# Kernel optimization log

Measured on AMD Instinct MI355X. Metric: run time of the kernel, lower is better.

The kernel has to match this reference:

```python
import jax, jax.numpy as jnp
import numpy as np

HEADS = 8
D_MODEL = 512
D_K = D_MODEL // HEADS
B, S = 2, 2048


def setup_inputs() -> dict:
    key = jax.random.key(0)
    ks = jax.random.split(key, 12)
    f = lambda k, shape: jax.random.normal(k, shape, dtype=jnp.float32)
    inp = {
        'q': f(ks[0], (B, S, D_MODEL)),
        'k': f(ks[1], (B, S, D_MODEL)),
        'v': f(ks[2], (B, S, D_MODEL)),
        'mask': jax.random.randint(ks[3], (B, S, S), 0, 2, dtype=jnp.int32),
        'Wq': f(ks[4], (D_MODEL, D_MODEL)) * 0.02,
        'bq': jnp.zeros((D_MODEL,), jnp.float32),
        'Wk': f(ks[5], (D_MODEL, D_MODEL)) * 0.02,
        'bk': jnp.zeros((D_MODEL,), jnp.float32),
        'Wv': f(ks[6], (D_MODEL, D_MODEL)) * 0.02,
        'bv': jnp.zeros((D_MODEL,), jnp.float32),
        'Wo': f(ks[7], (D_MODEL, D_MODEL)) * 0.02,
        'bo': jnp.zeros((D_MODEL,), jnp.float32),
    }
    return inp


def reference(q, k, v, mask, Wq, bq, Wk, bk, Wv, bv, Wo, bo):
    bs = q.shape[0]
    # linear projections then split heads: [B, H, S, D_K]
    qh = (q @ Wq + bq).reshape(bs, -1, HEADS, D_K).transpose(0, 2, 1, 3)
    kh = (k @ Wk + bk).reshape(bs, -1, HEADS, D_K).transpose(0, 2, 1, 3)
    vh = (v @ Wv + bv).reshape(bs, -1, HEADS, D_K).transpose(0, 2, 1, 3)
    # scores: [B, H, Sq, Sk]
    scores = jnp.einsum('bhqd,bhkd->bhqk', qh, kh) / jnp.sqrt(jnp.float32(D_K))
    scores = jnp.where(mask[:, None, :, :] == 0, jnp.float32(-10000.0), scores)
    attn = jax.nn.softmax(scores, axis=-1)
    # dropout p=0.0 -> identity (inference-equivalent)
    ctx = jnp.einsum('bhqk,bhkd->bhqd', attn, vh)
    concat = ctx.transpose(0, 2, 1, 3).reshape(bs, -1, D_MODEL)
    out = concat @ Wo + bo
    return (out, attn)
```

## Files before the change

### kernel.cpp

```cpp
#include <hip/hip_runtime.h>
#include <math.h>

#define HEADS 8
#define DK 64
#define DMODEL 512
#define BATCH 2
#define SEQ 2048
#define BH (BATCH * HEADS)

using f32x4 = __attribute__((ext_vector_type(4))) float;
using s16x8 = __attribute__((ext_vector_type(8))) short;
using fp16x2 = __attribute__((ext_vector_type(2))) __fp16;

union FragU {
  uint4 u;
  s16x8 s;
  unsigned short us[8];
};
union PkU {
  fp16x2 h;
  unsigned int u;
};

__device__ __forceinline__ unsigned short f32_to_bf16(float f) {
  unsigned int u = __float_as_uint(f);
  u += 0x7fffu + ((u >> 16) & 1u);
  return (unsigned short)(u >> 16);
}
__device__ __forceinline__ float bf16_to_f32(unsigned short h) {
  return __uint_as_float(((unsigned int)h) << 16);
}

__global__ __launch_bounds__(256) void pack_mask_kernel(
    const int* __restrict__ mask, unsigned int* __restrict__ bits) {
  const size_t row = blockIdx.x;
  const int wv = threadIdx.x >> 6, lane = threadIdx.x & 63;
  #pragma unroll
  for (int i = 0; i < 8; ++i) {
    const int c = wv * 512 + i * 64 + lane;
    unsigned long long bal = __ballot(mask[row * SEQ + c] != 0);
    if (lane == 0) {
      bits[row * 64 + (c >> 5)] = (unsigned int)bal;
      bits[row * 64 + (c >> 5) + 1] = (unsigned int)(bal >> 32);
    }
  }
}

__global__ __launch_bounds__(256) void wsplit4_kernel(
    const float* __restrict__ W0, const float* __restrict__ W1,
    const float* __restrict__ W2, const float* __restrict__ W3,
    unsigned short* __restrict__ WtHi4, unsigned short* __restrict__ WtLo4) {
  __shared__ float t[64][65];
  const int z = blockIdx.z;
  const float* W = (z == 0) ? W0 : (z == 1) ? W1 : (z == 2) ? W2 : W3;
  unsigned short* WtHi = WtHi4 + (size_t)z * (DMODEL * DMODEL);
  unsigned short* WtLo = WtLo4 + (size_t)z * (DMODEL * DMODEL);
  const int k0 = blockIdx.x * 64, n0 = blockIdx.y * 64;
  const int tid = threadIdx.x;
  const int r = tid >> 2, c = (tid & 3) * 16;
  #pragma unroll
  for (int e = 0; e < 4; ++e) {
    f32x4 v = *(const f32x4*)&W[(size_t)(k0 + r) * DMODEL + n0 + c + e * 4];
    #pragma unroll
    for (int j = 0; j < 4; ++j) t[r][c + e * 4 + j] = v[j];
  }
  __syncthreads();
  const int rn = tid >> 2, ck = (tid & 3) * 16;
  #pragma unroll
  for (int half = 0; half < 2; ++half) {
    FragU hi, lo;
    #pragma unroll
    for (int e = 0; e < 8; ++e) {
      float x = t[ck + half * 8 + e][rn];
      unsigned short h = f32_to_bf16(x);
      hi.us[e] = h;
      lo.us[e] = f32_to_bf16(x - bf16_to_f32(h));
    }
    const size_t o = (size_t)(n0 + rn) * DMODEL + k0 + ck + half * 8;
    *(uint4*)&WtHi[o] = hi.u;
    *(uint4*)&WtLo[o] = lo.u;
  }
}

template <int MODE>
__global__ __launch_bounds__(256) void proj_mfma_kernel(
    const float* __restrict__ X, const unsigned short* __restrict__ X16,
    const unsigned short* __restrict__ WtHi,
    const unsigned short* __restrict__ WtLo, const float* __restrict__ bias,
    float* __restrict__ Yf, unsigned short* __restrict__ Yhi,
    unsigned short* __restrict__ Ylo) {
  __shared__ unsigned short BsHi[64][72];
  __shared__ unsigned short BsLo[64][72];
  const int tid = threadIdx.x, wv = tid >> 6, lane = tid & 63;
  const int lr = lane & 15, lg = lane >> 4;
  const int m0 = blockIdx.x * 64;
  const int mw = m0 + wv * 16;
  const int n0 = blockIdx.y * 64;

  f32x4 acc[4] = {};
  for (int k0 = 0; k0 < 512; k0 += 64) {
    FragU ah[2], al[2];
    #pragma unroll
    for (int dc = 0; dc < 2; ++dc) {
      const size_t xi = (size_t)(mw + lr) * DMODEL + k0 + dc * 32 + lg * 8;
      if (MODE == 3) {
        ah[dc].u = *(const uint4*)&X16[xi];
      } else {
        f32x4 x0 = *(const f32x4*)&X[xi];
        f32x4 x1 = *(const f32x4*)&X[xi + 4];
        #pragma unroll
        for (int t = 0; t < 4; ++t) {
          unsigned short h0 = f32_to_bf16(x0[t]);
          unsigned short h1 = f32_to_bf16(x1[t]);
          ah[dc].us[t] = h0;
          ah[dc].us[4 + t] = h1;
          al[dc].us[t] = f32_to_bf16(x0[t] - bf16_to_f32(h0));
          al[dc].us[4 + t] = f32_to_bf16(x1[t] - bf16_to_f32(h1));
        }
      }
    }
    __syncthreads();
    #pragma unroll
    for (int e = 0; e < 2; ++e) {
      const int rr = (tid >> 3) + e * 32;
      const int cc = (tid & 7) * 8;
      *(uint4*)&BsHi[rr][cc] =
          *(const uint4*)&WtHi[(size_t)(n0 + rr) * DMODEL + k0 + cc];
      *(uint4*)&BsLo[rr][cc] =
          *(const uint4*)&WtLo[(size_t)(n0 + rr) * DMODEL + k0 + cc];
    }
    __syncthreads();
    #pragma unroll
    for (int jt = 0; jt < 4; ++jt) {
      #pragma unroll
      for (int dc = 0; dc < 2; ++dc) {
        FragU bh, bl;
        bh.u = *(const uint4*)&BsHi[jt * 16 + lr][dc * 32 + lg * 8];
        bl.u = *(const uint4*)&BsLo[jt * 16 + lr][dc * 32 + lg * 8];
        acc[jt] = __builtin_amdgcn_mfma_f32_16x16x32_bf16(ah[dc].s, bh.s, acc[jt], 0, 0, 0);
        acc[jt] = __builtin_amdgcn_mfma_f32_16x16x32_bf16(ah[dc].s, bl.s, acc[jt], 0, 0, 0);
        if (MODE != 3)
          acc[jt] = __builtin_amdgcn_mfma_f32_16x16x32_bf16(al[dc].s, bh.s, acc[jt], 0, 0, 0);
      }
    }
  }

  if (MODE == 3) {
    #pragma unroll
    for (int jt = 0; jt < 4; ++jt) {
      const int n = n0 + jt * 16 + lr;
      const float bi = bias[n];
      #pragma unroll
      for (int r = 0; r < 4; ++r)
        Yf[(size_t)(mw + lg * 4 + r) * DMODEL + n] = acc[jt][r] + bi;
    }
  } else {
    __syncthreads();
    #pragma unroll
    for (int jt = 0; jt < 4; ++jt) {
      const int n = jt * 16 + lr;
      const float bi = bias[n0 + n];
      #pragma unroll
      for (int r = 0; r < 4; ++r) {
        const float v = acc[jt][r] + bi;
        const int row = wv * 16 + lg * 4 + r;
        unsigned short hi = f32_to_bf16(v);
        BsHi[row][n] = hi;
        if (MODE == 1) BsLo[row][n] = f32_to_bf16(v - bf16_to_f32(hi));
      }
    }
    __syncthreads();
    if (MODE == 4) {
      const int b2 = m0 >> 11, s0 = m0 & 2047, hh = n0 >> 6;
      const int d = tid >> 2, sc = (tid & 3) * 16;
      #pragma unroll
      for (int e = 0; e < 16; ++e)
        Yhi[((size_t)(b2 * HEADS + hh) * DK + d) * SEQ + s0 + sc + e] =
            BsHi[sc + e][d];
    } else {
      #pragma unroll
      for (int p = 0; p < 2; ++p) {
        const int row = (tid >> 3) + p * 32;
        const int ch = (tid & 7) * 8;
        const size_t o = (size_t)(m0 + row) * DMODEL + n0 + ch;
        *(uint4*)&Yhi[o] = *(uint4*)&BsHi[row][ch];
        if (MODE == 1) *(uint4*)&Ylo[o] = *(uint4*)&BsLo[row][ch];
      }
    }
  }
}

__global__ __launch_bounds__(1024) void attn_fused_kernel(
    const unsigned short* __restrict__ Qhi, const unsigned short* __restrict__ Qlo,
    const unsigned short* __restrict__ Khi, const unsigned int* __restrict__ bits,
    const unsigned short* __restrict__ Vt, float* __restrict__ attn,
    unsigned short* __restrict__ ctx16) {
  __shared__ unsigned short pbuf[16][16 * 76];
  __shared__ float smred[16][16];
  const int id = blockIdx.x;
  const int xcd = id & 7, slot = id >> 3;
  const int bh = xcd + 8 * (slot & 1);
  const int qt = slot >> 1;
  const int b = bh >> 3, h = bh & 7;
  const int tid = threadIdx.x, wv = tid >> 6, lane = tid & 63;
  const int lr = lane & 15, lg = lane >> 4;
  const int q0 = qt * 16;
  const int kw = wv * 128;

  FragU qh[2], ql[2];
  #pragma unroll
  for (int dc = 0; dc < 2; ++dc) {
    const size_t qi = (size_t)(b * SEQ + q0 + lr) * DMODEL + h * DK + dc * 32 + lg * 8;
    qh[dc].u = *(const uint4*)&Qhi[qi];
    ql[dc].u = *(const uint4*)&Qlo[qi];
  }

  const float C = 0.125f * 1.44269504089f;
  PkU epk[8][2];
  float ls[4] = {0.f, 0.f, 0.f, 0.f};
  #pragma unroll
  for (int t = 0; t < 8; ++t) {
    FragU kh[2];
    #pragma unroll
    for (int dc = 0; dc < 2; ++dc) {
      const size_t kidx =
          (size_t)(b * SEQ + kw + t * 16 + lr) * DMODEL + h * DK + dc * 32 + lg * 8;
      kh[dc].u = *(const uint4*)&Khi[kidx];
    }
    f32x4 sa = {};
    #pragma unroll
    for (int dc = 0; dc < 2; ++dc) {
      sa = __builtin_amdgcn_mfma_f32_16x16x32_bf16(qh[dc].s, kh[dc].s, sa, 0, 0, 0);
      sa = __builtin_amdgcn_mfma_f32_16x16x32_bf16(ql[dc].s, kh[dc].s, sa, 0, 0, 0);
    }
    float ev[4];
    #pragma unroll
    for (int r = 0; r < 4; ++r) {
      const int q = q0 + lg * 4 + r;
      const unsigned int w = bits[((size_t)b * SEQ + q) * 64 + (kw >> 5) + (t >> 1)];
      const bool keep = (w >> (((t & 1) << 4) + lr)) & 1;
      const float e = keep ? exp2f(sa[r] * C) : 0.0f;
      ev[r] = e;
      ls[r] += e;
    }
    epk[t][0].h = __builtin_amdgcn_cvt_pkrtz(ev[0], ev[1]);
    epk[t][1].h = __builtin_amdgcn_cvt_pkrtz(ev[2], ev[3]);
  }

  #pragma unroll
  for (int r = 0; r < 4; ++r) {
    #pragma unroll
    for (int off = 1; off < 16; off <<= 1) ls[r] += __shfl_xor(ls[r], off);
    if (lr == 0) smred[wv][lg * 4 + r] = ls[r];
  }
  __syncthreads();
  float il[4];
  #pragma unroll
  for (int r = 0; r < 4; ++r) {
    float l = 0.f;
    #pragma unroll
    for (int w2 = 0; w2 < 16; ++w2) l += smred[w2][lg * 4 + r];
    il[r] = 1.0f / l;
  }

  unsigned short* pb = pbuf[wv];
  f32x4 acc[4] = {};
  #pragma unroll
  for (int c = 0; c < 2; ++c) {
    #pragma unroll
    for (int tt = 0; tt < 4; ++tt) {
      const int t = c * 4 + tt;
      float pv4[4];
      pv4[0] = (float)epk[t][0].h.x * il[0];
      pv4[1] = (float)epk[t][0].h.y * il[1];
      pv4[2] = (float)epk[t][1].h.x * il[2];
      pv4[3] = (float)epk[t][1].h.y * il[3];
      #pragma unroll
      for (int r = 0; r < 4; ++r) {
        const int q = q0 + lg * 4 + r;
        __builtin_nontemporal_store(
            pv4[r], &attn[((size_t)bh * SEQ + q) * SEQ + kw + t * 16 + lr]);
        pb[(lg * 4 + r) * 76 + tt * 16 + lr] = f32_to_bf16(pv4[r]);
      }
    }
    #pragma unroll
    for (int dc2 = 0; dc2 < 2; ++dc2) {
      FragU pa;
      pa.u = *(const uint4*)&pb[lr * 76 + dc2 * 32 + lg * 8];
      #pragma unroll
      for (int dt = 0; dt < 4; ++dt) {
        FragU bv;
        bv.u = *(const uint4*)&Vt[((size_t)bh * DK + dt * 16 + lr) * SEQ + kw +
                                  c * 64 + dc2 * 32 + lg * 8];
        acc[dt] = __builtin_amdgcn_mfma_f32_16x16x32_bf16(pa.s, bv.s, acc[dt], 0, 0, 0);
      }
    }
  }

  float* red = (float*)&pbuf[0][0];
  #pragma unroll 1
  for (int ofs = 8; ofs > 0; ofs >>= 1) {
    __syncthreads();
    if (wv >= ofs && wv < 2 * ofs) {
      float* dst = red + (size_t)(wv - ofs) * 1024;
      #pragma unroll
      for (int dt = 0; dt < 4; ++dt) *(f32x4*)&dst[dt * 256 + lane * 4] = acc[dt];
    }
    __syncthreads();
    if (wv < ofs) {
      const float* src = red + (size_t)wv * 1024;
      #pragma unroll
      for (int dt = 0; dt < 4; ++dt) acc[dt] += *(const f32x4*)&src[dt * 256 + lane * 4];
    }
  }
  if (wv == 0) {
    #pragma unroll
    for (int dt = 0; dt < 4; ++dt)
      #pragma unroll
      for (int r = 0; r < 4; ++r) {
        const int q = q0 + lg * 4 + r;
        ctx16[(size_t)(b * SEQ + q) * DMODEL + h * DK + dt * 16 + lr] =
            f32_to_bf16(acc[dt][r]);
      }
  }
}

extern "C" void kernel_launch(void* const* d_in, const int* in_sizes, int n_in,
                              void* d_out, int out_size, void* d_ws,
                              size_t ws_size, hipStream_t stream) {
  const float* q = (const float*)d_in[0];
  const float* k = (const float*)d_in[1];
  const float* v = (const float*)d_in[2];
  const int* mask = (const int*)d_in[3];
  const float* Wq = (const float*)d_in[4];
  const float* bq = (const float*)d_in[5];
  const float* Wk = (const float*)d_in[6];
  const float* bk = (const float*)d_in[7];
  const float* Wv = (const float*)d_in[8];
  const float* bv = (const float*)d_in[9];
  const float* Wo = (const float*)d_in[10];
  const float* bo = (const float*)d_in[11];

  float* out = (float*)d_out;
  float* attn = out + (size_t)BATCH * SEQ * DMODEL;

  char* w = (char*)d_ws;
  const size_t MB = 1u << 20;
  unsigned short* Qhi = (unsigned short*)(w + 0 * MB);
  unsigned short* Qlo = (unsigned short*)(w + 4 * MB);
  unsigned short* Khi = (unsigned short*)(w + 8 * MB);
  unsigned short* WtHi4 = (unsigned short*)(w + 12 * MB);
  unsigned short* WtLo4 = (unsigned short*)(w + 14 * MB);
  unsigned short* ctx16 = (unsigned short*)(w + 16 * MB);
  unsigned short* Vt = (unsigned short*)(w + 20 * MB);
  unsigned int* bits = (unsigned int*)(w + 24 * MB);

  const size_t WSTRIDE = (size_t)DMODEL * DMODEL;

  dim3 blk(256);
  pack_mask_kernel<<<dim3(BATCH * SEQ), blk, 0, stream>>>(mask, bits);

  wsplit4_kernel<<<dim3(8, 8, 4), blk, 0, stream>>>(Wq, Wk, Wv, Wo, WtHi4, WtLo4);

  proj_mfma_kernel<1><<<dim3(64, 8), blk, 0, stream>>>(
      q, nullptr, WtHi4 + 0 * WSTRIDE, WtLo4 + 0 * WSTRIDE, bq, nullptr, Qhi, Qlo);
  proj_mfma_kernel<2><<<dim3(64, 8), blk, 0, stream>>>(
      k, nullptr, WtHi4 + 1 * WSTRIDE, WtLo4 + 1 * WSTRIDE, bk, nullptr, Khi, nullptr);
  proj_mfma_kernel<4><<<dim3(64, 8), blk, 0, stream>>>(
      v, nullptr, WtHi4 + 2 * WSTRIDE, WtLo4 + 2 * WSTRIDE, bv, nullptr, Vt, nullptr);

  attn_fused_kernel<<<dim3(2048), dim3(1024), 0, stream>>>(Qhi, Qlo, Khi, bits,
                                                           Vt, attn, ctx16);

  proj_mfma_kernel<3><<<dim3(64, 8), blk, 0, stream>>>(
      nullptr, ctx16, WtHi4 + 3 * WSTRIDE, WtLo4 + 3 * WSTRIDE, bo, out, nullptr, nullptr);
}
```

Measured before the change: 251.1 us.

## Merge Q/K/V projections into one launch, preload mask words, use plain attn stores

The three separate Q, K and V projection launches become a single kernel that picks its input, weights and output layout from blockIdx.z. This removes two launches and lets the three projections fill the GPU together. In the attention kernel, each lane now loads its four mask words as one uint4 up front instead of issuing a scalar load per tile. The attention-probability stores switch from nontemporal to ordinary stores, which may change how the large attn write interacts with the cache.

Result: no change. 250.6 us, median of 2 (-0.2%).

```diff
diff --git a/kernel.cpp b/kernel.cpp
--- a/kernel.cpp
+++ b/kernel.cpp
@@ -82,13 +82,109 @@
   }
 }
 
-template <int MODE>
-__global__ __launch_bounds__(256) void proj_mfma_kernel(
-    const float* __restrict__ X, const unsigned short* __restrict__ X16,
-    const unsigned short* __restrict__ WtHi,
+__global__ __launch_bounds__(256) void proj_qkv_kernel(
+    const float* __restrict__ Xq, const float* __restrict__ Xk,
+    const float* __restrict__ Xv, const unsigned short* __restrict__ WtHi4,
+    const unsigned short* __restrict__ WtLo4, const float* __restrict__ bq,
+    const float* __restrict__ bk, const float* __restrict__ bv,
+    unsigned short* __restrict__ Qhi, unsigned short* __restrict__ Qlo,
+    unsigned short* __restrict__ Khi, unsigned short* __restrict__ Vt) {
+  __shared__ unsigned short BsHi[64][72];
+  __shared__ unsigned short BsLo[64][72];
+  const int z = blockIdx.z;
+  const float* X = (z == 0) ? Xq : (z == 1) ? Xk : Xv;
+  const float* bias = (z == 0) ? bq : (z == 1) ? bk : bv;
+  const unsigned short* WtHi = WtHi4 + (size_t)z * (DMODEL * DMODEL);
+  const unsigned short* WtLo = WtLo4 + (size_t)z * (DMODEL * DMODEL);
+
+  const int tid = threadIdx.x, wv = tid >> 6, lane = tid & 63;
+  const int lr = lane & 15, lg = lane >> 4;
+  const int m0 = blockIdx.x * 64;
+  const int mw = m0 + wv * 16;
+  const int n0 = blockIdx.y * 64;
+
+  f32x4 acc[4] = {};
+  for (int k0 = 0; k0 < 512; k0 += 64) {
+    FragU ah[2], al[2];
+    #pragma unroll
+    for (int dc = 0; dc < 2; ++dc) {
+      const size_t xi = (size_t)(mw + lr) * DMODEL + k0 + dc * 32 + lg * 8;
+      f32x4 x0 = *(const f32x4*)&X[xi];
+      f32x4 x1 = *(const f32x4*)&X[xi + 4];
+      #pragma unroll
+      for (int t = 0; t < 4; ++t) {
+        unsigned short h0 = f32_to_bf16(x0[t]);
+        unsigned short h1 = f32_to_bf16(x1[t]);
+        ah[dc].us[t] = h0;
+        ah[dc].us[4 + t] = h1;
+        al[dc].us[t] = f32_to_bf16(x0[t] - bf16_to_f32(h0));
+        al[dc].us[4 + t] = f32_to_bf16(x1[t] - bf16_to_f32(h1));
+      }
+    }
+    __syncthreads();
+    #pragma unroll
+    for (int e = 0; e < 2; ++e) {
+      const int rr = (tid >> 3) + e * 32;
+      const int cc = (tid & 7) * 8;
+      *(uint4*)&BsHi[rr][cc] =
+          *(const uint4*)&WtHi[(size_t)(n0 + rr) * DMODEL + k0 + cc];
+      *(uint4*)&BsLo[rr][cc] =
+          *(const uint4*)&WtLo[(size_t)(n0 + rr) * DMODEL + k0 + cc];
+    }
+    __syncthreads();
+    #pragma unroll
+    for (int jt = 0; jt < 4; ++jt) {
+      #pragma unroll
+      for (int dc = 0; dc < 2; ++dc) {
+        FragU bh, bl;
+        bh.u = *(const uint4*)&BsHi[jt * 16 + lr][dc * 32 + lg * 8];
+        bl.u = *(const uint4*)&BsLo[jt * 16 + lr][dc * 32 + lg * 8];
+        acc[jt] = __builtin_amdgcn_mfma_f32_16x16x32_bf16(ah[dc].s, bh.s, acc[jt], 0, 0, 0);
+        acc[jt] = __builtin_amdgcn_mfma_f32_16x16x32_bf16(ah[dc].s, bl.s, acc[jt], 0, 0, 0);
+        acc[jt] = __builtin_amdgcn_mfma_f32_16x16x32_bf16(al[dc].s, bh.s, acc[jt], 0, 0, 0);
+      }
+    }
+  }
+
+  __syncthreads();
+  #pragma unroll
+  for (int jt = 0; jt < 4; ++jt) {
+    const int n = jt * 16 + lr;
+    const float bi = bias[n0 + n];
+    #pragma unroll
+    for (int r = 0; r < 4; ++r) {
+      const float v = acc[jt][r] + bi;
+      const int row = wv * 16 + lg * 4 + r;
+      unsigned short hi = f32_to_bf16(v);
+      BsHi[row][n] = hi;
+      if (z == 0) BsLo[row][n] = f32_to_bf16(v - bf16_to_f32(hi));
+    }
+  }
+  __syncthreads();
+  if (z == 2) {
+    const int b2 = m0 >> 11, s0 = m0 & 2047, hh = n0 >> 6;
+    const int d = tid >> 2, sc = (tid & 3) * 16;
+    #pragma unroll
+    for (int e = 0; e < 16; ++e)
+      Vt[((size_t)(b2 * HEADS + hh) * DK + d) * SEQ + s0 + sc + e] =
+          BsHi[sc + e][d];
+  } else {
+    unsigned short* Yhi = (z == 0) ? Qhi : Khi;
+    #pragma unroll
+    for (int p = 0; p < 2; ++p) {
+      const int row = (tid >> 3) + p * 32;
+      const int ch = (tid & 7) * 8;
+      const size_t o = (size_t)(m0 + row) * DMODEL + n0 + ch;
+      *(uint4*)&Yhi[o] = *(uint4*)&BsHi[row][ch];
+      if (z == 0) *(uint4*)&Qlo[o] = *(uint4*)&BsLo[row][ch];
+    }
+  }
+}
+
+__global__ __launch_bounds__(256) void proj_out_kernel(
+    const unsigned short* __restrict__ X16, const unsigned short* __restrict__ WtHi,
     const unsigned short* __restrict__ WtLo, const float* __restrict__ bias,
-    float* __restrict__ Yf, unsigned short* __restrict__ Yhi,
-    unsigned short* __restrict__ Ylo) {
+    float* __restrict__ Yf) {
   __shared__ unsigned short BsHi[64][72];
   __shared__ unsigned short BsLo[64][72];
   const int tid = threadIdx.x, wv = tid >> 6, lane = tid & 63;
@@ -99,25 +195,11 @@
 
   f32x4 acc[4] = {};
   for (int k0 = 0; k0 < 512; k0 += 64) {
-    FragU ah[2], al[2];
+    FragU ah[2];
     #pragma unroll
     for (int dc = 0; dc < 2; ++dc) {
       const size_t xi = (size_t)(mw + lr) * DMODEL + k0 + dc * 32 + lg * 8;
-      if (MODE == 3) {
-        ah[dc].u = *(const uint4*)&X16[xi];
-      } else {
-        f32x4 x0 = *(const f32x4*)&X[xi];
-        f32x4 x1 = *(const f32x4*)&X[xi + 4];
-        #pragma unroll
-        for (int t = 0; t < 4; ++t) {
-          unsigned short h0 = f32_to_bf16(x0[t]);
-          unsigned short h1 = f32_to_bf16(x1[t]);
-          ah[dc].us[t] = h0;
-          ah[dc].us[4 + t] = h1;
-          al[dc].us[t] = f32_to_bf16(x0[t] - bf16_to_f32(h0));
-          al[dc].us[4 + t] = f32_to_bf16(x1[t] - bf16_to_f32(h1));
-        }
-      }
+      ah[dc].u = *(const uint4*)&X16[xi];
     }
     __syncthreads();
     #pragma unroll
@@ -139,54 +221,16 @@
         bl.u = *(const uint4*)&BsLo[jt * 16 + lr][dc * 32 + lg * 8];
         acc[jt] = __builtin_amdgcn_mfma_f32_16x16x32_bf16(ah[dc].s, bh.s, acc[jt], 0, 0, 0);
         acc[jt] = __builtin_amdgcn_mfma_f32_16x16x32_bf16(ah[dc].s, bl.s, acc[jt], 0, 0, 0);
-        if (MODE != 3)
-          acc[jt] = __builtin_amdgcn_mfma_f32_16x16x32_bf16(al[dc].s, bh.s, acc[jt], 0, 0, 0);
-      }
-    }
-  }
-
-  if (MODE == 3) {
-    #pragma unroll
-    for (int jt = 0; jt < 4; ++jt) {
-      const int n = n0 + jt * 16 + lr;
-      const float bi = bias[n];
-      #pragma unroll
-      for (int r = 0; r < 4; ++r)
-        Yf[(size_t)(mw + lg * 4 + r) * DMODEL + n] = acc[jt][r] + bi;
-    }
-  } else {
-    __syncthreads();
-    #pragma unroll
-    for (int jt = 0; jt < 4; ++jt) {
-      const int n = jt * 16 + lr;
-      const float bi = bias[n0 + n];
-      #pragma unroll
-      for (int r = 0; r < 4; ++r) {
-        const float v = acc[jt][r] + bi;
-        const int row = wv * 16 + lg * 4 + r;
-        unsigned short hi = f32_to_bf16(v);
-        BsHi[row][n] = hi;
-        if (MODE == 1) BsLo[row][n] = f32_to_bf16(v - bf16_to_f32(hi));
-      }
-    }
-    __syncthreads();
-    if (MODE == 4) {
-      const int b2 = m0 >> 11, s0 = m0 & 2047, hh = n0 >> 6;
-      const int d = tid >> 2, sc = (tid & 3) * 16;
-      #pragma unroll
-      for (int e = 0; e < 16; ++e)
-        Yhi[((size_t)(b2 * HEADS + hh) * DK + d) * SEQ + s0 + sc + e] =
-            BsHi[sc + e][d];
-    } else {
-      #pragma unroll
-      for (int p = 0; p < 2; ++p) {
-        const int row = (tid >> 3) + p * 32;
-        const int ch = (tid & 7) * 8;
-        const size_t o = (size_t)(m0 + row) * DMODEL + n0 + ch;
-        *(uint4*)&Yhi[o] = *(uint4*)&BsHi[row][ch];
-        if (MODE == 1) *(uint4*)&Ylo[o] = *(uint4*)&BsLo[row][ch];
-      }
-    }
+      }
+    }
+  }
+  #pragma unroll
+  for (int jt = 0; jt < 4; ++jt) {
+    const int n = n0 + jt * 16 + lr;
+    const float bi = bias[n];
+    #pragma unroll
+    for (int r = 0; r < 4; ++r)
+      Yf[(size_t)(mw + lg * 4 + r) * DMODEL + n] = acc[jt][r] + bi;
   }
 }
 
@@ -214,6 +258,12 @@
     qh[dc].u = *(const uint4*)&Qhi[qi];
     ql[dc].u = *(const uint4*)&Qlo[qi];
   }
+  uint4 mw4[4];
+  #pragma unroll
+  for (int r = 0; r < 4; ++r) {
+    const int q = q0 + lg * 4 + r;
+    mw4[r] = *(const uint4*)&bits[((size_t)b * SEQ + q) * 64 + (kw >> 5)];
+  }
 
   const float C = 0.125f * 1.44269504089f;
   PkU epk[8][2];
@@ -236,8 +286,9 @@
     float ev[4];
     #pragma unroll
     for (int r = 0; r < 4; ++r) {
-      const int q = q0 + lg * 4 + r;
-      const unsigned int w = bits[((size_t)b * SEQ + q) * 64 + (kw >> 5) + (t >> 1)];
+      const unsigned int w =
+          (t >> 1) == 0 ? mw4[r].x : (t >> 1) == 1 ? mw4[r].y
+          : (t >> 1) == 2 ? mw4[r].z : mw4[r].w;
       const bool keep = (w >> (((t & 1) << 4) + lr)) & 1;
       const float e = keep ? exp2f(sa[r] * C) : 0.0f;
       ev[r] = e;
@@ -278,8 +329,7 @@
       #pragma unroll
       for (int r = 0; r < 4; ++r) {
         const int q = q0 + lg * 4 + r;
-        __builtin_nontemporal_store(
-            pv4[r], &attn[((size_t)bh * SEQ + q) * SEQ + kw + t * 16 + lr]);
+        attn[((size_t)bh * SEQ + q) * SEQ + kw + t * 16 + lr] = pv4[r];
         pb[(lg * 4 + r) * 76 + tt * 16 + lr] = f32_to_bf16(pv4[r]);
       }
     }
@@ -362,16 +412,12 @@
 
   wsplit4_kernel<<<dim3(8, 8, 4), blk, 0, stream>>>(Wq, Wk, Wv, Wo, WtHi4, WtLo4);
 
-  proj_mfma_kernel<1><<<dim3(64, 8), blk, 0, stream>>>(
-      q, nullptr, WtHi4 + 0 * WSTRIDE, WtLo4 + 0 * WSTRIDE, bq, nullptr, Qhi, Qlo);
-  proj_mfma_kernel<2><<<dim3(64, 8), blk, 0, stream>>>(
-      k, nullptr, WtHi4 + 1 * WSTRIDE, WtLo4 + 1 * WSTRIDE, bk, nullptr, Khi, nullptr);
-  proj_mfma_kernel<4><<<dim3(64, 8), blk, 0, stream>>>(
-      v, nullptr, WtHi4 + 2 * WSTRIDE, WtLo4 + 2 * WSTRIDE, bv, nullptr, Vt, nullptr);
+  proj_qkv_kernel<<<dim3(64, 8, 3), blk, 0, stream>>>(
+      q, k, v, WtHi4, WtLo4, bq, bk, bv, Qhi, Qlo, Khi, Vt);
 
   attn_fused_kernel<<<dim3(2048), dim3(1024), 0, stream>>>(Qhi, Qlo, Khi, bits,
                                                            Vt, attn, ctx16);
 
-  proj_mfma_kernel<3><<<dim3(64, 8), blk, 0, stream>>>(
-      nullptr, ctx16, WtHi4 + 3 * WSTRIDE, WtLo4 + 3 * WSTRIDE, bo, out, nullptr, nullptr);
-}
+  proj_out_kernel<<<dim3(64, 8), blk, 0, stream>>>(
+      ctx16, WtHi4 + 3 * WSTRIDE, WtLo4 + 3 * WSTRIDE, bo, out);
+}
```
